# Kernel optimization log

Measured on AMD Instinct MI355X. Metric: run time of the kernel, lower is better.

## Reference

```python
import jax, jax.numpy as jnp
import numpy as np

N_SEARCH, B, C, H, W = 10, 32, 768, 24, 24
HT, WT = 8, 8
HEADS, POOL = 12, 4


def _G(t):
    # Integral of the bilinear triangle kernel: G(t) = int_{-1}^{t} max(0,1-|s|) ds
    tc = jnp.clip(t, -1.0, 1.0)
    return 0.5 + tc * (1.0 - 0.5 * jnp.abs(tc))


def prroi_pool(feats, rois, pool):
    # feats: [R,C,H,W], rois: [R,4] pixel coords (x0,y0,x1,y1); exact PrRoIPool2D
    R, C_, H_, W_ = feats.shape
    x0, y0, x1, y1 = rois[:, 0], rois[:, 1], rois[:, 2], rois[:, 3]
    bw = (x1 - x0) / pool
    bh = (y1 - y0) / pool
    p = jnp.arange(pool, dtype=feats.dtype)
    ex0 = x0[:, None] + p[None, :] * bw[:, None]   # [R,pool]
    ex1 = ex0 + bw[:, None]
    ey0 = y0[:, None] + p[None, :] * bh[:, None]
    ey1 = ey0 + bh[:, None]
    ix = jnp.arange(W_, dtype=feats.dtype)
    iy = jnp.arange(H_, dtype=feats.dtype)
    wx = _G(ex1[:, :, None] - ix) - _G(ex0[:, :, None] - ix)  # [R,pool,W]
    wy = _G(ey1[:, :, None] - iy) - _G(ey0[:, :, None] - iy)  # [R,pool,H]
    area = jnp.maximum(bw * bh, 1e-8)[:, None, None, None]
    return jnp.einsum('rph,rqw,rchw->rcpq', wy, wx, feats) / area  # [R,C,pool,pool]


def layernorm(x, g, b, eps=1e-5):
    m = jnp.mean(x, -1, keepdims=True)
    v = jnp.mean((x - m) ** 2, -1, keepdims=True)
    return (x - m) * jax.lax.rsqrt(v + eps) * g + b


def setup_inputs():
    key = jax.random.key(0)
    ks = jax.random.split(key, 24)
    search_feats = jax.random.normal(ks[0], (N_SEARCH, B, C, H, W), jnp.float32)
    template_feat = jax.random.normal(ks[1], (N_SEARCH, B, C, HT, WT), jnp.float32)
    u = jax.random.uniform(ks[2], (N_SEARCH, B, 4), jnp.float32)
    x0 = 0.05 + 0.4 * u[..., 0]
    y0 = 0.05 + 0.4 * u[..., 1]
    x1 = x0 + 0.15 + 0.3 * u[..., 2]
    y1 = y0 + 0.15 + 0.3 * u[..., 3]
    search_boxes = jnp.stack([x0, y0, x1, y1], -1)  # normalized, x1>x0, y1>y0
    s = 0.02
    d = {
        'search_feats': search_feats,
        'template_feat': template_feat,
        'search_boxes': search_boxes,
        'score_token': s * jax.random.normal(ks[3], (1, 1, C), jnp.float32),
        'ln1_g': jnp.ones((C,), jnp.float32), 'ln1_b': jnp.zeros((C,), jnp.float32),
        'Wq': s * jax.random.normal(ks[4], (2, C, C), jnp.float32), 'bq': jnp.zeros((2, C), jnp.float32),
        'Wk': s * jax.random.normal(ks[5], (2, C, C), jnp.float32), 'bk': jnp.zeros((2, C), jnp.float32),
        'Wv': s * jax.random.normal(ks[6], (2, C, C), jnp.float32), 'bv': jnp.zeros((2, C), jnp.float32),
        'Wo': s * jax.random.normal(ks[7], (2, C, C), jnp.float32), 'bo': jnp.zeros((2, C), jnp.float32),
        'ln2_g': jnp.ones((2, C), jnp.float32), 'ln2_b': jnp.zeros((2, C), jnp.float32),
        'Wmix': s * jax.random.normal(ks[8], (2, N_SEARCH, N_SEARCH), jnp.float32),
        'bmix': jnp.zeros((2, N_SEARCH), jnp.float32),
        'W1': s * jax.random.normal(ks[9], (C, C), jnp.float32), 'b1': jnp.zeros((C,), jnp.float32),
        'W2': s * jax.random.normal(ks[10], (C, C), jnp.float32), 'b2': jnp.zeros((C,), jnp.float32),
        'W3': s * jax.random.normal(ks[11], (C, 1), jnp.float32), 'b3': jnp.zeros((1,), jnp.float32),
    }
    return d


def reference(search_feats, template_feat, search_boxes, score_token, ln1_g, ln1_b,
              Wq, bq, Wk, bk, Wv, bv, Wo, bo, ln2_g, ln2_b, Wmix, bmix,
              W1, b1, W2, b2, W3, b3):
    N, b, c, h, w = search_feats.shape
    heads, pool = HEADS, POOL
    dh = c // heads
    scale = c ** (-0.5)  # note: full hidden_dim scale, as in original

    boxes = (search_boxes * w).reshape(-1, 4)              # [N*b,4] pixel coords
    feats = search_feats.reshape(-1, c, h, w)              # [N*b,c,h,w]
    pooled = prroi_pool(feats, boxes, pool)                # [N*b,c,pool,pool]
    # 'b c h w -> b (h w) c' then split N
    sbf = pooled.reshape(N, b, c, pool * pool).transpose(0, 1, 3, 2)  # [N,b,16,c]
    tmpl = template_feat.reshape(N, b, c, -1).transpose(0, 1, 3, 2)   # [N,b,64,c]

    x = jnp.broadcast_to(score_token, (N, b, 1, c))
    x = layernorm(x, ln1_g, ln1_b)
    kv = [sbf, tmpl]
    for i in range(2):
        q = x @ Wq[i] + bq[i]                              # [N,b,1,c]
        k = kv[i] @ Wk[i] + bk[i]                          # [N,b,T,c]
        v = kv[i] @ Wv[i] + bv[i]
        T = k.shape[2]
        qh = q.reshape(N, b, 1, heads, dh).transpose(0, 1, 3, 2, 4)   # [N,b,H,1,d]
        kh = k.reshape(N, b, T, heads, dh).transpose(0, 1, 3, 2, 4)   # [N,b,H,T,d]
        vh = v.reshape(N, b, T, heads, dh).transpose(0, 1, 3, 2, 4)
        attn = jax.nn.softmax(jnp.einsum('nbhld,nbhtd->nbhlt', qh, kh) * scale, -1)
        o = jnp.einsum('nbhlt,nbhtd->nbhld', attn, vh)
        o = o.transpose(0, 1, 3, 2, 4).reshape(N, b, 1, c)
        o = layernorm(o @ Wo[i] + bo[i], ln2_g[i], ln2_b[i])
        # time-mix across the N frames: [N,b,1,c] -> [b,c,N] -> linear -> [N,b,1,c]
        t = o[:, :, 0, :].transpose(1, 2, 0)               # [b,c,N]
        t = t @ Wmix[i] + bmix[i]
        x = t.transpose(2, 0, 1)[:, :, None, :]            # [N,b,1,c]

    hdd = jax.nn.relu(x @ W1 + b1)
    hdd = jax.nn.relu(hdd @ W2 + b2)
    return hdd @ W3 + b3                                   # [N,b,1,1]
```

## Files before the change

### kernel.cpp

```cpp
#include <hip/hip_runtime.h>
#include <cstdint>
#include <cstddef>

namespace {

constexpr float kScale = 0.03608439182435161f;
constexpr float kEps   = 1e-5f;

constexpr size_t OFF_QK0T = 0;
constexpr size_t OFF_QBK0 = 9216;
constexpr size_t OFF_S    = 16384;
constexpr size_t OFF_QK1  = OFF_S   + 2949120;
constexpr size_t OFF_O    = OFF_QK1 + 2949120;
constexpr size_t OFF_U    = OFF_O   + 245760;
constexpr size_t OFF_X    = OFF_U   + 245760;
constexpr size_t OFF_QF1  = OFF_X   + 245760;
constexpr size_t OFF_H1   = OFF_QF1 + 245760;
constexpr size_t OFF_H2   = OFF_H1  + 245760;
constexpr size_t OFF_WF   = OFF_H2  + 245760;
constexpr size_t WF_MAT_SHORTS = 1179648;
constexpr size_t OFF_P    = OFF_WF + (7*WF_MAT_SHORTS)/2;

typedef short short8v __attribute__((ext_vector_type(8)));
typedef float float4v __attribute__((ext_vector_type(4)));

union BP  { int4 i4; short8v s8; };
union S4P { int2 i2; short s[4]; };

__device__ __forceinline__ void splitBf(float a, short &h, short &l){
    unsigned u = __float_as_uint(a);
    h = (short)(u >> 16);
    float r = a - __uint_as_float(u & 0xFFFF0000u);
    l = (short)(__float_as_uint(r) >> 16);
}

__device__ __forceinline__ float Gf(float t){
    float tc = fminf(fmaxf(t, -1.f), 1.f);
    return 0.5f + tc * (1.f - 0.5f * fabsf(tc));
}

__device__ __forceinline__ float blockReduce256(float v, float* red){
    #pragma unroll
    for (int off = 1; off < 64; off <<= 1) v += __shfl_xor(v, off);
    __syncthreads();
    if ((threadIdx.x & 63) == 0) red[threadIdx.x >> 6] = v;
    __syncthreads();
    return red[0] + red[1] + red[2] + red[3];
}

__global__ __launch_bounds__(256) void k_wprep(
        const float* __restrict__ w0, const float* __restrict__ w1,
        const float* __restrict__ w2, const float* __restrict__ w3,
        const float* __restrict__ w4, const float* __restrict__ w5,
        const float* __restrict__ w6, short* __restrict__ WF){
    const float* Wsel[7] = {w0,w1,w2,w3,w4,w5,w6};
    const float* W = Wsel[blockIdx.y];
    const int unit = blockIdx.x * 4 + (threadIdx.x >> 6);
    const int l = threadIdx.x & 63;
    const int kt = unit / 48, nb = unit % 48;
    const int n = nb*16 + (l & 15);
    const int kb = kt*32 + ((l >> 4) << 2);
    S4P hi0, hi1, lo0, lo1;
    #pragma unroll
    for (int e = 0; e < 4; ++e){
        float a = W[(size_t)(kb + e) * 768 + n];
        splitBf(a, hi0.s[e], lo0.s[e]);
        float b = W[(size_t)(kb + 16 + e) * 768 + n];
        splitBf(b, hi1.s[e], lo1.s[e]);
    }
    size_t base = (size_t)blockIdx.y * WF_MAT_SHORTS + (size_t)unit * 1024 + (size_t)l * 8;
    *(int2*)(WF + base)            = hi0.i2;
    *(int2*)(WF + base + 4)        = hi1.i2;
    *(int2*)(WF + base + 512)      = lo0.i2;
    *(int2*)(WF + base + 512 + 4)  = lo1.i2;
}

template<int HG, int RELU>
__global__ __launch_bounds__(256) void k_mgemm(
        const float* __restrict__ A, const short* __restrict__ WFm,
        const float* __restrict__ bias, float* __restrict__ C){
    __shared__ short AF[2][2][64][8];
    const int h   = blockIdx.y;
    const int m0  = blockIdx.x * 16;
    const int tid = threadIdx.x;
    const int l   = tid & 63;
    const int w   = tid >> 6;

    const int srow = tid >> 3, sk4 = tid & 7;
    const int slane = srow + 16 * (sk4 & 3);
    const int sebase = 4 * (sk4 >> 2);
    const float* aRow = HG ? (A + ((size_t)(m0 + srow) * 12 + h) * 768)
                           : (A + (size_t)(m0 + srow) * 768);

    const int nb = h * 4 + w;
    const short* WB = WFm + (size_t)nb * 1024 + (size_t)l * 8;

    float4v acc = {0.f,0.f,0.f,0.f};

    if (tid < 128){
        float4 a0 = *(const float4*)(aRow + sk4 * 4);
        S4P hi, lo;
        splitBf(a0.x, hi.s[0], lo.s[0]); splitBf(a0.y, hi.s[1], lo.s[1]);
        splitBf(a0.z, hi.s[2], lo.s[2]); splitBf(a0.w, hi.s[3], lo.s[3]);
        *(int2*)&AF[0][0][slane][sebase] = hi.i2;
        *(int2*)&AF[0][1][slane][sebase] = lo.i2;
    }
    BP bh, bl;
    bh.i4 = *(const int4*)(WB);
    bl.i4 = *(const int4*)(WB + 512);
    __syncthreads();

    #pragma unroll 1
    for (int kt = 0; kt < 24; ++kt){
        const int cur = kt & 1;
        const int ktn = (kt < 23) ? kt + 1 : 23;
        float4 aN;
        if (tid < 128) aN = *(const float4*)(aRow + ktn * 32 + sk4 * 4);
        BP cbh = bh, cbl = bl;
        {
            const short* wb = WB + (size_t)ktn * 49152;
            bh.i4 = *(const int4*)(wb);
            bl.i4 = *(const int4*)(wb + 512);
        }
        short8v ah = *(short8v*)&AF[cur][0][l][0];
        short8v al = *(short8v*)&AF[cur][1][l][0];
        acc = __builtin_amdgcn_mfma_f32_16x16x32_bf16(ah, cbh.s8, acc, 0, 0, 0);
        acc = __builtin_amdgcn_mfma_f32_16x16x32_bf16(al, cbh.s8, acc, 0, 0, 0);
        acc = __builtin_amdgcn_mfma_f32_16x16x32_bf16(ah, cbl.s8, acc, 0, 0, 0);
        if (kt < 23 && tid < 128){
            S4P hi, lo;
            splitBf(aN.x, hi.s[0], lo.s[0]); splitBf(aN.y, hi.s[1], lo.s[1]);
            splitBf(aN.z, hi.s[2], lo.s[2]); splitBf(aN.w, hi.s[3], lo.s[3]);
            *(int2*)&AF[cur ^ 1][0][slane][sebase] = hi.i2;
            *(int2*)&AF[cur ^ 1][1][slane][sebase] = lo.i2;
        }
        __syncthreads();
    }

    const int col = h * 64 + w * 16 + (l & 15);
    const float bb = bias[col];
    #pragma unroll
    for (int reg = 0; reg < 4; ++reg){
        int row = m0 + ((l >> 4) << 2) + reg;
        float v = acc[reg] + bb;
        if (RELU) v = fmaxf(v, 0.f);
        C[(size_t)row * 768 + col] = v;
    }
}

__global__ __launch_bounds__(256) void k_prep(
        const float* __restrict__ token, const float* __restrict__ g1,
        const float* __restrict__ b1,    const float* __restrict__ Wq0,
        const float* __restrict__ bq0,   const float* __restrict__ Wk0,
        const float* __restrict__ bk0,
        float* __restrict__ qk0T, float* __restrict__ qbk0){
    __shared__ float x0l[768];
    __shared__ float red[8];
    __shared__ float qfp[4][64];
    __shared__ float qfl[64];
    __shared__ float Ws[64][68];
    const int h  = blockIdx.x / 12;
    const int ct = blockIdx.x % 12;
    const int tid = threadIdx.x;

    float v0 = token[tid], v1 = token[tid+256], v2 = token[tid+512];
    float s = blockReduce256(v0+v1+v2, red);
    float m = s * (1.f/768.f);
    float d0 = v0-m, d1 = v1-m, d2 = v2-m;
    float qv = blockReduce256(d0*d0+d1*d1+d2*d2, red);
    float rs = rsqrtf(qv*(1.f/768.f) + kEps);
    x0l[tid]     = d0*rs*g1[tid]     + b1[tid];
    x0l[tid+256] = d1*rs*g1[tid+256] + b1[tid+256];
    x0l[tid+512] = d2*rs*g1[tid+512] + b1[tid+512];
    __syncthreads();

    {
        int dl = tid & 63, part = tid >> 6;
        int d = h*64 + dl;
        float a = 0.f;
        for (int c = part*192; c < part*192 + 192; ++c)
            a += x0l[c] * Wq0[(size_t)c*768 + d];
        qfp[part][dl] = a;
    }
    __syncthreads();
    if (tid < 64){
        int d = h*64 + tid;
        qfl[tid] = qfp[0][tid]+qfp[1][tid]+qfp[2][tid]+qfp[3][tid] + bq0[d];
    }
    __syncthreads();
    if (ct == 0 && tid < 64){
        float v = qfl[tid] * bk0[h*64 + tid];
        #pragma unroll
        for (int off = 1; off < 64; off <<= 1) v += __shfl_xor(v, off);
        if (tid == 0) qbk0[h] = v;
    }
    #pragma unroll
    for (int i = 0; i < 4; ++i){
        int f = tid + i*256; int cl = f >> 4, dd = (f & 15)*4;
        float4 v = *(const float4*)(Wk0 + (size_t)(ct*64+cl)*768 + h*64 + dd);
        *(float4*)&Ws[cl][dd] = v;
    }
    __syncthreads();
    {
        int cl = tid >> 2, part = tid & 3;
        float a = 0.f;
        #pragma unroll
        for (int jj = 0; jj < 16; ++jj){
            int dd = part*16 + jj;
            a += Ws[cl][dd] * qfl[dd];
        }
        a += __shfl_xor(a, 1); a += __shfl_xor(a, 2);
        if (part == 0) qk0T[h*768 + ct*64 + cl] = a;
    }
}

__global__ __launch_bounds__(256) void k_pool2(
        const float* __restrict__ feats, const float* __restrict__ boxes,
        float* __restrict__ P){
    __shared__ float Xs[32*580];
    __shared__ float wxp[24][4];
    __shared__ float wyp[24][4];
    __shared__ int   rng[2];
    __shared__ float areaInvS;
    const int r = blockIdx.x, cc = blockIdx.y * 32, tid = threadIdx.x;

    float bx0 = boxes[r*4+0]*24.f, by0 = boxes[r*4+1]*24.f;
    float bx1 = boxes[r*4+2]*24.f, by1 = boxes[r*4+3]*24.f;
    float bw = (bx1-bx0)*0.25f, bh = (by1-by0)*0.25f;
    if (tid == 0){
        int hlo = (int)floorf(by0) - 1; if (hlo < 0) hlo = 0;
        int hhi = (int)floorf(by1) + 1; if (hhi > 23) hhi = 23;
        rng[0] = hlo; rng[1] = hhi - hlo + 1;
        areaInvS = 1.f / fmaxf(bw*bh, 1e-8f);
    }
    if (tid < 24){
        int w = tid;
        #pragma unroll
        for (int q = 0; q < 4; ++q){
            float e0 = bx0 + q*bw, e1 = e0 + bw;
            wxp[w][q] = Gf(e1 - (float)w) - Gf(e0 - (float)w);
        }
    } else if (tid < 48){
        int hh = tid - 24;
        #pragma unroll
        for (int p = 0; p < 4; ++p){
            float e0 = by0 + p*bh, e1 = e0 + bh;
            wyp[hh][p] = Gf(e1 - (float)hh) - Gf(e0 - (float)hh);
        }
    }
    __syncthreads();
    const int hlo = rng[0], nr = rng[1];
    const float aInv = areaInvS;

    const int nf4 = nr * 192;
    for (int idx = tid; idx < nf4; idx += 256){
        int ri  = idx / 192;
        int rem = idx - ri * 192;
        int cl  = rem / 6;
        int w4  = rem - cl * 6;
        float4 v = *(const float4*)(feats + ((size_t)(r*768 + cc + cl))*576
                                    + (hlo + ri)*24 + w4*4);
        *(float4*)&Xs[cl*580 + ri*24 + w4*4] = v;
    }
    __syncthreads();

    const int j = tid & 7;
    const int cl = tid >> 3;
    float acc[16];
    #pragma unroll
    for (int k = 0; k < 16; ++k) acc[k] = 0.f;
    for (int ri = j; ri < nr; ri += 8){
        const float* xr = &Xs[cl*580 + ri*24];
        float z[4] = {0.f,0.f,0.f,0.f};
        #pragma unroll
        for (int w4 = 0; w4 < 6; ++w4){
            float4 xv = *(const float4*)(xr + w4*4);
            float xa[4] = {xv.x, xv.y, xv.z, xv.w};
            #pragma unroll
            for (int k = 0; k < 4; ++k){
                float4 wv = *(const float4*)&wxp[w4*4+k][0];
                z[0] += wv.x*xa[k]; z[1] += wv.y*xa[k];
                z[2] += wv.z*xa[k]; z[3] += wv.w*xa[k];
            }
        }
        float4 wyv = *(const float4*)&wyp[hlo+ri][0];
        float wya[4] = {wyv.x, wyv.y, wyv.z, wyv.w};
        #pragma unroll
        for (int p = 0; p < 4; ++p)
            #pragma unroll
            for (int q = 0; q < 4; ++q)
                acc[p*4+q] += wya[p]*z[q];
    }
    #pragma unroll
    for (int k = 0; k < 16; ++k){
        acc[k] += __shfl_xor(acc[k], 1);
        acc[k] += __shfl_xor(acc[k], 2);
        acc[k] += __shfl_xor(acc[k], 4);
    }
    float o0 = acc[0], o1 = acc[8];
    #pragma unroll
    for (int k = 1; k < 8; ++k){
        if (j == k){ o0 = acc[k]; o1 = acc[k+8]; }
    }
    P[((size_t)r*16 + j)*768 + cc + cl]     = o0 * aInv;
    P[((size_t)r*16 + j + 8)*768 + cc + cl] = o1 * aInv;
}

__global__ __launch_bounds__(256) void k_attn0(
        const float* __restrict__ P, const float* __restrict__ qk0T,
        const float* __restrict__ qbk0g, float* __restrict__ s0){
    __shared__ float P2[16][776];
    __shared__ float logitsL[12][17];
    __shared__ float attnT[16][12];
    const int r = blockIdx.x, tid = threadIdx.x;

    #pragma unroll
    for (int i = 0; i < 12; ++i){
        int f = tid + i*256;
        int t = f / 192, c4 = f - t*192;
        float4 v = *(const float4*)(P + ((size_t)r*16 + t)*768 + c4*4);
        *(float4*)&P2[t][c4*4] = v;
    }
    __syncthreads();

    if (tid < 192){
        int h = tid >> 4, t = tid & 15;
        float a = qbk0g[h];
        const float* qrow = qk0T + h*768;
        #pragma unroll 4
        for (int c4 = 0; c4 < 192; ++c4){
            float4 qv = *(const float4*)(qrow + c4*4);
            float4 pv = *(const float4*)&P2[t][c4*4];
            a += qv.x*pv.x + qv.y*pv.y + qv.z*pv.z + qv.w*pv.w;
        }
        logitsL[h][t] = a * kScale;
    }
    __syncthreads();
    if (tid < 12){
        float mx = -1e30f;
        for (int t = 0; t < 16; ++t) mx = fmaxf(mx, logitsL[tid][t]);
        float ss = 0.f;
        for (int t = 0; t < 16; ++t){
            float e = expf(logitsL[tid][t] - mx);
            attnT[t][tid] = e; ss += e;
        }
        float rsn = 1.f/ss;
        for (int t = 0; t < 16; ++t) attnT[t][tid] *= rsn;
    }
    __syncthreads();
    #pragma unroll
    for (int s3 = 0; s3 < 3; ++s3){
        int c = tid + s3*256;
        float a12[12];
        #pragma unroll
        for (int h = 0; h < 12; ++h) a12[h] = 0.f;
        #pragma unroll
        for (int t = 0; t < 16; ++t){
            float x = P2[t][c];
            float4 a0 = *(const float4*)&attnT[t][0];
            float4 a1 = *(const float4*)&attnT[t][4];
            float4 a2 = *(const float4*)&attnT[t][8];
            a12[0] += a0.x*x; a12[1] += a0.y*x; a12[2]  += a0.z*x; a12[3]  += a0.w*x;
            a12[4] += a1.x*x; a12[5] += a1.y*x; a12[6]  += a1.z*x; a12[7]  += a1.w*x;
            a12[8] += a2.x*x; a12[9] += a2.y*x; a12[10] += a2.z*x; a12[11] += a2.w*x;
        }
        #pragma unroll
        for (int h = 0; h < 12; ++h)
            s0[((size_t)r*12 + h)*768 + c] = a12[h];
    }
}

__global__ __launch_bounds__(256) void k_qk1(
        const float* __restrict__ qf1, const float* __restrict__ Wk1,
        float* __restrict__ qk1){
    __shared__ float As[32][68];
    __shared__ float Bs[64][68];
    const int r0 = blockIdx.x * 32, h = blockIdx.y, c0 = blockIdx.z * 64;
    const int tid = threadIdx.x;
    #pragma unroll
    for (int i = 0; i < 2; ++i){
        int f = tid + i*256; int ml = f >> 4, kk = (f & 15)*4;
        *(float4*)&As[ml][kk] =
            *(const float4*)(qf1 + (size_t)(r0+ml)*768 + h*64 + kk);
    }
    #pragma unroll
    for (int i = 0; i < 4; ++i){
        int f = tid + i*256; int cl = f >> 4, dd = (f & 15)*4;
        float4 v = *(const float4*)(Wk1 + (size_t)(c0+cl)*768 + h*64 + dd);
        Bs[dd+0][cl] = v.x; Bs[dd+1][cl] = v.y;
        Bs[dd+2][cl] = v.z; Bs[dd+3][cl] = v.w;
    }
    __syncthreads();
    const int tn = tid & 15, tm = tid >> 4;
    float acc0[4] = {0.f,0.f,0.f,0.f};
    float acc1[4] = {0.f,0.f,0.f,0.f};
    #pragma unroll
    for (int k4 = 0; k4 < 16; ++k4){
        float4 av0 = *(const float4*)&As[tm*2+0][k4*4];
        float4 av1 = *(const float4*)&As[tm*2+1][k4*4];
        float a0a[4] = {av0.x, av0.y, av0.z, av0.w};
        float a1a[4] = {av1.x, av1.y, av1.z, av1.w};
        #pragma unroll
        for (int jj = 0; jj < 4; ++jj){
            float4 bv = *(const float4*)&Bs[k4*4+jj][tn*4];
            acc0[0] += a0a[jj]*bv.x; acc0[1] += a0a[jj]*bv.y;
            acc0[2] += a0a[jj]*bv.z; acc0[3] += a0a[jj]*bv.w;
            acc1[0] += a1a[jj]*bv.x; acc1[1] += a1a[jj]*bv.y;
            acc1[2] += a1a[jj]*bv.z; acc1[3] += a1a[jj]*bv.w;
        }
    }
    float4 o0; o0.x=acc0[0]; o0.y=acc0[1]; o0.z=acc0[2]; o0.w=acc0[3];
    float4 o1; o1.x=acc1[0]; o1.y=acc1[1]; o1.z=acc1[2]; o1.w=acc1[3];
    *(float4*)(qk1 + ((size_t)(r0+tm*2+0)*12 + h)*768 + c0 + tn*4) = o0;
    *(float4*)(qk1 + ((size_t)(r0+tm*2+1)*12 + h)*768 + c0 + tn*4) = o1;
}

__global__ __launch_bounds__(256) void k_attn1(
        const float* __restrict__ tmpl, const float* __restrict__ qf1,
        const float* __restrict__ bk1,  const float* __restrict__ qk1,
        float* __restrict__ s1){
    __shared__ float Tc[192][68];
    __shared__ float logitsT[64][13];
    __shared__ float attnH[12][64];
    __shared__ float qbk[12];
    const int r = blockIdx.x, tid = threadIdx.x;
    const float* tp = tmpl + (size_t)r*768*64;

    if (tid < 192){
        int h = tid >> 4, pp = tid & 15;
        float v = 0.f;
        #pragma unroll
        for (int jj = 0; jj < 4; ++jj){
            int d = h*64 + pp*4 + jj;
            v += bk1[d] * qf1[(size_t)r*768 + d];
        }
        v += __shfl_xor(v,1); v += __shfl_xor(v,2);
        v += __shfl_xor(v,4); v += __shfl_xor(v,8);
        if (pp == 0) qbk[h] = v;
    }
    __syncthreads();
    float lacc[3];
    #pragma unroll
    for (int s = 0; s < 3; ++s){
        int task = tid + s*256;
        lacc[s] = qbk[task >> 6];
    }
    for (int cb = 0; cb < 4; ++cb){
        #pragma unroll
        for (int i = 0; i < 12; ++i){
            int f = tid + i*256; int cl = f >> 4, t4 = (f & 15)*4;
            *(float4*)&Tc[cl][t4] =
                *(const float4*)(tp + (size_t)(cb*192 + cl)*64 + t4);
        }
        __syncthreads();
        #pragma unroll
        for (int s = 0; s < 3; ++s){
            int task = tid + s*256;
            int h = task >> 6, t = task & 63;
            const float* qrow = qk1 + ((size_t)r*12 + h)*768 + cb*192;
            float a = 0.f;
            #pragma unroll 4
            for (int c4 = 0; c4 < 48; ++c4){
                float4 qv = *(const float4*)(qrow + c4*4);
                a += qv.x*Tc[c4*4+0][t] + qv.y*Tc[c4*4+1][t]
                   + qv.z*Tc[c4*4+2][t] + qv.w*Tc[c4*4+3][t];
            }
            lacc[s] += a;
        }
        __syncthreads();
    }
    #pragma unroll
    for (int s = 0; s < 3; ++s){
        int task = tid + s*256;
        logitsT[task & 63][task >> 6] = lacc[s] * kScale;
    }
    __syncthreads();
    if (tid < 12){
        float mx = -1e30f;
        for (int t = 0; t < 64; ++t) mx = fmaxf(mx, logitsT[t][tid]);
        float ss = 0.f;
        for (int t = 0; t < 64; ++t){
            float e = expf(logitsT[t][tid] - mx);
            attnH[tid][t] = e; ss += e;
        }
        float rsn = 1.f/ss;
        for (int t = 0; t < 64; ++t) attnH[tid][t] *= rsn;
    }
    __syncthreads();
    for (int cb = 0; cb < 4; ++cb){
        #pragma unroll
        for (int i = 0; i < 12; ++i){
            int f = tid + i*256; int cl = f >> 4, t4 = (f & 15)*4;
            *(float4*)&Tc[cl][t4] =
                *(const float4*)(tp + (size_t)(cb*192 + cl)*64 + t4);
        }
        __syncthreads();
        if (tid < 192){
            float4 trow[16];
            #pragma unroll
            for (int t4 = 0; t4 < 16; ++t4)
                trow[t4] = *(const float4*)&Tc[tid][t4*4];
            int c = cb*192 + tid;
            #pragma unroll
            for (int h = 0; h < 12; ++h){
                float a = 0.f;
                #pragma unroll
                for (int t4 = 0; t4 < 16; ++t4){
                    float4 avv = *(const float4*)&attnH[h][t4*4];
                    float4 tv = trow[t4];
                    a += avv.x*tv.x + avv.y*tv.y + avv.z*tv.z + avv.w*tv.w;
                }
                s1[((size_t)r*12 + h)*768 + c] = a;
            }
        }
        __syncthreads();
    }
}

__global__ __launch_bounds__(256) void k_lnmix(
        const float* __restrict__ u, const float* __restrict__ g,
        const float* __restrict__ bta, const float* __restrict__ Wmix,
        const float* __restrict__ bmix, float* __restrict__ xout){
    __shared__ float lnl[10][768];
    __shared__ float red[8];
    __shared__ float wm[100];
    __shared__ float bm[10];
    const int b = blockIdx.x, tid = threadIdx.x;
    if (tid < 100) wm[tid] = Wmix[tid];
    if (tid < 10)  bm[tid] = bmix[tid];
    for (int n = 0; n < 10; ++n){
        const float* row = u + (size_t)(n*32 + b)*768;
        float v0 = row[tid], v1 = row[tid+256], v2 = row[tid+512];
        float s = blockReduce256(v0+v1+v2, red);
        float m = s * (1.f/768.f);
        float d0 = v0-m, d1 = v1-m, d2 = v2-m;
        float qv = blockReduce256(d0*d0+d1*d1+d2*d2, red);
        float rs = rsqrtf(qv*(1.f/768.f) + kEps);
        lnl[n][tid]     = d0*rs*g[tid]     + bta[tid];
        lnl[n][tid+256] = d1*rs*g[tid+256] + bta[tid+256];
        lnl[n][tid+512] = d2*rs*g[tid+512] + bta[tid+512];
    }
    __syncthreads();
    #pragma unroll
    for (int s3 = 0; s3 < 3; ++s3){
        int c = tid + s3*256;
        float col[10];
        #pragma unroll
        for (int n = 0; n < 10; ++n) col[n] = lnl[n][c];
        #pragma unroll
        for (int np = 0; np < 10; ++np){
            float a = bm[np];
            #pragma unroll
            for (int n = 0; n < 10; ++n) a += col[n]*wm[n*10+np];
            xout[(size_t)(np*32 + b)*768 + c] = a;
        }
    }
}

__global__ __launch_bounds__(256) void k_head(
        const float* __restrict__ h2v, const float* __restrict__ W3,
        const float* __restrict__ b3, float* __restrict__ out){
    __shared__ float red[8];
    const int r = blockIdx.x, tid = threadIdx.x;
    const float* row = h2v + (size_t)r*768;
    float a = row[tid]*W3[tid] + row[tid+256]*W3[tid+256] + row[tid+512]*W3[tid+512];
    a = blockReduce256(a, red);
    if (tid == 0) out[r] = a + b3[0];
}

}

extern "C" void kernel_launch(void* const* d_in, const int* in_sizes, int n_in,
                              void* d_out, int out_size, void* d_ws, size_t ws_size,
                              hipStream_t stream){
    const float* feats = (const float*)d_in[0];
    const float* tmpl  = (const float*)d_in[1];
    const float* boxes = (const float*)d_in[2];
    const float* token = (const float*)d_in[3];
    const float* ln1g  = (const float*)d_in[4];
    const float* ln1b  = (const float*)d_in[5];
    const float* Wq    = (const float*)d_in[6];
    const float* bq    = (const float*)d_in[7];
    const float* Wk    = (const float*)d_in[8];
    const float* bk    = (const float*)d_in[9];
    const float* Wv    = (const float*)d_in[10];
    const float* bv    = (const float*)d_in[11];
    const float* Wo    = (const float*)d_in[12];
    const float* bo    = (const float*)d_in[13];
    const float* ln2g  = (const float*)d_in[14];
    const float* ln2b  = (const float*)d_in[15];
    const float* Wmix  = (const float*)d_in[16];
    const float* bmix  = (const float*)d_in[17];
    const float* W1    = (const float*)d_in[18];
    const float* b1v   = (const float*)d_in[19];
    const float* W2    = (const float*)d_in[20];
    const float* b2v   = (const float*)d_in[21];
    const float* W3    = (const float*)d_in[22];
    const float* b3v   = (const float*)d_in[23];
    float* ws  = (float*)d_ws;
    float* out = (float*)d_out;

    float* qk0T = ws + OFF_QK0T;
    float* qbk0 = ws + OFF_QBK0;
    float* sbuf = ws + OFF_S;
    float* qk1  = ws + OFF_QK1;
    float* obuf = ws + OFF_O;
    float* ubuf = ws + OFF_U;
    float* xbuf = ws + OFF_X;
    float* qf1  = ws + OFF_QF1;
    float* h1b  = ws + OFF_H1;
    float* h2b  = ws + OFF_H2;
    short* wf   = (short*)(ws + OFF_WF);
    float* Pbuf = ws + OFF_P;

    const size_t MO = 589824;
    short* wfv0 = wf + 0*WF_MAT_SHORTS;
    short* wfo0 = wf + 1*WF_MAT_SHORTS;
    short* wfq1 = wf + 2*WF_MAT_SHORTS;
    short* wfv1 = wf + 3*WF_MAT_SHORTS;
    short* wfo1 = wf + 4*WF_MAT_SHORTS;
    short* wf1  = wf + 5*WF_MAT_SHORTS;
    short* wf2  = wf + 6*WF_MAT_SHORTS;

    k_wprep<<<dim3(288,7), 256, 0, stream>>>(Wv, Wo, Wq + MO, Wv + MO, Wo + MO, W1, W2, wf);
    k_prep<<<144, 256, 0, stream>>>(token, ln1g, ln1b, Wq, bq, Wk, bk, qk0T, qbk0);
    k_pool2<<<dim3(320,24), 256, 0, stream>>>(feats, boxes, Pbuf);
    k_attn0<<<320, 256, 0, stream>>>(Pbuf, qk0T, qbk0, sbuf);
    k_mgemm<1,0><<<dim3(20,12), 256, 0, stream>>>(sbuf, wfv0, bv, obuf);
    k_mgemm<0,0><<<dim3(20,12), 256, 0, stream>>>(obuf, wfo0, bo, ubuf);
    k_lnmix<<<32, 256, 0, stream>>>(ubuf, ln2g, ln2b, Wmix, bmix, xbuf);
    k_mgemm<0,0><<<dim3(20,12), 256, 0, stream>>>(xbuf, wfq1, bq + 768, qf1);
    k_qk1<<<dim3(10,12,12), 256, 0, stream>>>(qf1, Wk + MO, qk1);
    k_attn1<<<320, 256, 0, stream>>>(tmpl, qf1, bk + 768, qk1, sbuf);
    k_mgemm<1,0><<<dim3(20,12), 256, 0, stream>>>(sbuf, wfv1, bv + 768, obuf);
    k_mgemm<0,0><<<dim3(20,12), 256, 0, stream>>>(obuf, wfo1, bo + 768, ubuf);
    k_lnmix<<<32, 256, 0, stream>>>(ubuf, ln2g + 768, ln2b + 768, Wmix + 100, bmix + 10, xbuf);
    k_mgemm<0,1><<<dim3(20,12), 256, 0, stream>>>(xbuf, wf1, b1v, h1b);
    k_mgemm<0,1><<<dim3(20,12), 256, 0, stream>>>(h1b, wf2, b2v, h2b);
    k_head<<<320, 256, 0, stream>>>(h2b, W3, b3v, out);
}
```

Before: 404.3 us.

## Merge weight prep with token prep, retile mgemm, shrink pool2 LDS

Fuses the weight-splitting kernel and the token/query prep kernel into one launch that dispatches on block index. The split-bf16 GEMM is retiled to 32 rows per block with 8 waves and a K-step of 64, halving the grid and sharing each weight fragment across two row tiles. pool2 now stages rows in chunks of 12 instead of the full window, which cuts LDS per block for occupancy at the cost of extra barriers. Together these target launch overhead, weight re-reads and LDS-limited occupancy.

After: 363.3 us. 1.11x faster.

```diff
diff --git a/kernel.cpp b/kernel.cpp
--- a/kernel.cpp
+++ b/kernel.cpp
@@ -48,107 +48,11 @@
     return red[0] + red[1] + red[2] + red[3];
 }
 
-__global__ __launch_bounds__(256) void k_wprep(
+__global__ __launch_bounds__(256) void k_prepall(
         const float* __restrict__ w0, const float* __restrict__ w1,
         const float* __restrict__ w2, const float* __restrict__ w3,
         const float* __restrict__ w4, const float* __restrict__ w5,
-        const float* __restrict__ w6, short* __restrict__ WF){
-    const float* Wsel[7] = {w0,w1,w2,w3,w4,w5,w6};
-    const float* W = Wsel[blockIdx.y];
-    const int unit = blockIdx.x * 4 + (threadIdx.x >> 6);
-    const int l = threadIdx.x & 63;
-    const int kt = unit / 48, nb = unit % 48;
-    const int n = nb*16 + (l & 15);
-    const int kb = kt*32 + ((l >> 4) << 2);
-    S4P hi0, hi1, lo0, lo1;
-    #pragma unroll
-    for (int e = 0; e < 4; ++e){
-        float a = W[(size_t)(kb + e) * 768 + n];
-        splitBf(a, hi0.s[e], lo0.s[e]);
-        float b = W[(size_t)(kb + 16 + e) * 768 + n];
-        splitBf(b, hi1.s[e], lo1.s[e]);
-    }
-    size_t base = (size_t)blockIdx.y * WF_MAT_SHORTS + (size_t)unit * 1024 + (size_t)l * 8;
-    *(int2*)(WF + base)            = hi0.i2;
-    *(int2*)(WF + base + 4)        = hi1.i2;
-    *(int2*)(WF + base + 512)      = lo0.i2;
-    *(int2*)(WF + base + 512 + 4)  = lo1.i2;
-}
-
-template<int HG, int RELU>
-__global__ __launch_bounds__(256) void k_mgemm(
-        const float* __restrict__ A, const short* __restrict__ WFm,
-        const float* __restrict__ bias, float* __restrict__ C){
-    __shared__ short AF[2][2][64][8];
-    const int h   = blockIdx.y;
-    const int m0  = blockIdx.x * 16;
-    const int tid = threadIdx.x;
-    const int l   = tid & 63;
-    const int w   = tid >> 6;
-
-    const int srow = tid >> 3, sk4 = tid & 7;
-    const int slane = srow + 16 * (sk4 & 3);
-    const int sebase = 4 * (sk4 >> 2);
-    const float* aRow = HG ? (A + ((size_t)(m0 + srow) * 12 + h) * 768)
-                           : (A + (size_t)(m0 + srow) * 768);
-
-    const int nb = h * 4 + w;
-    const short* WB = WFm + (size_t)nb * 1024 + (size_t)l * 8;
-
-    float4v acc = {0.f,0.f,0.f,0.f};
-
-    if (tid < 128){
-        float4 a0 = *(const float4*)(aRow + sk4 * 4);
-        S4P hi, lo;
-        splitBf(a0.x, hi.s[0], lo.s[0]); splitBf(a0.y, hi.s[1], lo.s[1]);
-        splitBf(a0.z, hi.s[2], lo.s[2]); splitBf(a0.w, hi.s[3], lo.s[3]);
-        *(int2*)&AF[0][0][slane][sebase] = hi.i2;
-        *(int2*)&AF[0][1][slane][sebase] = lo.i2;
-    }
-    BP bh, bl;
-    bh.i4 = *(const int4*)(WB);
-    bl.i4 = *(const int4*)(WB + 512);
-    __syncthreads();
-
-    #pragma unroll 1
-    for (int kt = 0; kt < 24; ++kt){
-        const int cur = kt & 1;
-        const int ktn = (kt < 23) ? kt + 1 : 23;
-        float4 aN;
-        if (tid < 128) aN = *(const float4*)(aRow + ktn * 32 + sk4 * 4);
-        BP cbh = bh, cbl = bl;
-        {
-            const short* wb = WB + (size_t)ktn * 49152;
-            bh.i4 = *(const int4*)(wb);
-            bl.i4 = *(const int4*)(wb + 512);
-        }
-        short8v ah = *(short8v*)&AF[cur][0][l][0];
-        short8v al = *(short8v*)&AF[cur][1][l][0];
-        acc = __builtin_amdgcn_mfma_f32_16x16x32_bf16(ah, cbh.s8, acc, 0, 0, 0);
-        acc = __builtin_amdgcn_mfma_f32_16x16x32_bf16(al, cbh.s8, acc, 0, 0, 0);
-        acc = __builtin_amdgcn_mfma_f32_16x16x32_bf16(ah, cbl.s8, acc, 0, 0, 0);
-        if (kt < 23 && tid < 128){
-            S4P hi, lo;
-            splitBf(aN.x, hi.s[0], lo.s[0]); splitBf(aN.y, hi.s[1], lo.s[1]);
-            splitBf(aN.z, hi.s[2], lo.s[2]); splitBf(aN.w, hi.s[3], lo.s[3]);
-            *(int2*)&AF[cur ^ 1][0][slane][sebase] = hi.i2;
-            *(int2*)&AF[cur ^ 1][1][slane][sebase] = lo.i2;
-        }
-        __syncthreads();
-    }
-
-    const int col = h * 64 + w * 16 + (l & 15);
-    const float bb = bias[col];
-    #pragma unroll
-    for (int reg = 0; reg < 4; ++reg){
-        int row = m0 + ((l >> 4) << 2) + reg;
-        float v = acc[reg] + bb;
-        if (RELU) v = fmaxf(v, 0.f);
-        C[(size_t)row * 768 + col] = v;
-    }
-}
-
-__global__ __launch_bounds__(256) void k_prep(
+        const float* __restrict__ w6, short* __restrict__ WF,
         const float* __restrict__ token, const float* __restrict__ g1,
         const float* __restrict__ b1,    const float* __restrict__ Wq0,
         const float* __restrict__ bq0,   const float* __restrict__ Wk0,
@@ -159,9 +63,38 @@
     __shared__ float qfp[4][64];
     __shared__ float qfl[64];
     __shared__ float Ws[64][68];
-    const int h  = blockIdx.x / 12;
-    const int ct = blockIdx.x % 12;
+    const int gb = blockIdx.x;
     const int tid = threadIdx.x;
+    const int l = tid & 63;
+
+    if (gb < 2016){
+        const float* Wsel[7] = {w0,w1,w2,w3,w4,w5,w6};
+        const int mat = gb / 288;
+        const int bxx = gb - mat*288;
+        const float* W = Wsel[mat];
+        const int unit = bxx * 4 + (tid >> 6);
+        const int kt = unit / 48, nb = unit % 48;
+        const int n = nb*16 + (l & 15);
+        const int kb = kt*32 + ((l >> 4) << 2);
+        S4P hi0, hi1, lo0, lo1;
+        #pragma unroll
+        for (int e = 0; e < 4; ++e){
+            float a = W[(size_t)(kb + e) * 768 + n];
+            splitBf(a, hi0.s[e], lo0.s[e]);
+            float b = W[(size_t)(kb + 16 + e) * 768 + n];
+            splitBf(b, hi1.s[e], lo1.s[e]);
+        }
+        size_t base = (size_t)mat * WF_MAT_SHORTS + (size_t)unit * 1024 + (size_t)l * 8;
+        *(int2*)(WF + base)            = hi0.i2;
+        *(int2*)(WF + base + 4)        = hi1.i2;
+        *(int2*)(WF + base + 512)      = lo0.i2;
+        *(int2*)(WF + base + 512 + 4)  = lo1.i2;
+        return;
+    }
+
+    const int pb = gb - 2016;
+    const int h  = pb / 12;
+    const int ct = pb % 12;
 
     float v0 = token[tid], v1 = token[tid+256], v2 = token[tid+512];
     float s = blockReduce256(v0+v1+v2, red);
@@ -214,10 +147,96 @@
     }
 }
 
+template<int HG, int RELU>
+__global__ __launch_bounds__(512) void k_mgemm(
+        const float* __restrict__ A, const short* __restrict__ WFm,
+        const float* __restrict__ bias, float* __restrict__ C){
+    __shared__ short AF[2][2][2][2][64][8];
+    const int h   = blockIdx.y;
+    const int m0  = blockIdx.x * 32;
+    const int tid = threadIdx.x;
+    const int l   = tid & 63;
+    const int w   = tid >> 6;
+    const int wm  = w >> 2, wn = w & 3;
+
+    const int srow = tid >> 4;
+    const int sk4  = tid & 15;
+    const int sfs  = sk4 >> 3;
+    const int ss   = sk4 & 7;
+    const int sfm  = srow >> 4;
+    const int slane = (srow & 15) + 16 * (ss & 3);
+    const int seb   = 4 * (ss >> 2);
+    const float* aRow = HG ? (A + ((size_t)(m0 + srow) * 12 + h) * 768)
+                           : (A + (size_t)(m0 + srow) * 768);
+
+    const int nb = h * 4 + wn;
+    const short* WB = WFm + (size_t)nb * 1024 + (size_t)l * 8;
+
+    float4v acc = {0.f,0.f,0.f,0.f};
+
+    {
+        float4 a0 = *(const float4*)(aRow + sk4 * 4);
+        S4P hi, lo;
+        splitBf(a0.x, hi.s[0], lo.s[0]); splitBf(a0.y, hi.s[1], lo.s[1]);
+        splitBf(a0.z, hi.s[2], lo.s[2]); splitBf(a0.w, hi.s[3], lo.s[3]);
+        *(int2*)&AF[0][sfs][sfm][0][slane][seb] = hi.i2;
+        *(int2*)&AF[0][sfs][sfm][1][slane][seb] = lo.i2;
+    }
+    BP bh0, bl0, bh1, bl1;
+    bh0.i4 = *(const int4*)(WB);
+    bl0.i4 = *(const int4*)(WB + 512);
+    bh1.i4 = *(const int4*)(WB + 49152);
+    bl1.i4 = *(const int4*)(WB + 49152 + 512);
+    __syncthreads();
+
+    #pragma unroll 1
+    for (int kt = 0; kt < 12; ++kt){
+        const int cur = kt & 1;
+        float4 aN;
+        if (kt < 11) aN = *(const float4*)(aRow + (kt+1) * 64 + sk4 * 4);
+        BP cbh0 = bh0, cbl0 = bl0, cbh1 = bh1, cbl1 = bl1;
+        if (kt < 11){
+            const short* wb = WB + (size_t)(2*kt + 2) * 49152;
+            bh0.i4 = *(const int4*)(wb);
+            bl0.i4 = *(const int4*)(wb + 512);
+            bh1.i4 = *(const int4*)(wb + 49152);
+            bl1.i4 = *(const int4*)(wb + 49152 + 512);
+        }
+        short8v ah0 = *(short8v*)&AF[cur][0][wm][0][l][0];
+        short8v al0 = *(short8v*)&AF[cur][0][wm][1][l][0];
+        short8v ah1 = *(short8v*)&AF[cur][1][wm][0][l][0];
+        short8v al1 = *(short8v*)&AF[cur][1][wm][1][l][0];
+        acc = __builtin_amdgcn_mfma_f32_16x16x32_bf16(ah0, cbh0.s8, acc, 0, 0, 0);
+        acc = __builtin_amdgcn_mfma_f32_16x16x32_bf16(al0, cbh0.s8, acc, 0, 0, 0);
+        acc = __builtin_amdgcn_mfma_f32_16x16x32_bf16(ah0, cbl0.s8, acc, 0, 0, 0);
+        acc = __builtin_amdgcn_mfma_f32_16x16x32_bf16(ah1, cbh1.s8, acc, 0, 0, 0);
+        acc = __builtin_amdgcn_mfma_f32_16x16x32_bf16(al1, cbh1.s8, acc, 0, 0, 0);
+        acc = __builtin_amdgcn_mfma_f32_16x16x32_bf16(ah1, cbl1.s8, acc, 0, 0, 0);
+        if (kt < 11){
+            S4P hi, lo;
+            splitBf(aN.x, hi.s[0], lo.s[0]); splitBf(aN.y, hi.s[1], lo.s[1]);
+            splitBf(aN.z, hi.s[2], lo.s[2]); splitBf(aN.w, hi.s[3], lo.s[3]);
+            *(int2*)&AF[cur ^ 1][sfs][sfm][0][slane][seb] = hi.i2;
+            *(int2*)&AF[cur ^ 1][sfs][sfm][1][slane][seb] = lo.i2;
+        }
+        __syncthreads();
+    }
+
+    const int col = h * 64 + wn * 16 + (l & 15);
+    const float bb = bias[col];
+    #pragma unroll
+    for (int reg = 0; reg < 4; ++reg){
+        int row = m0 + wm * 16 + ((l >> 4) << 2) + reg;
+        float v = acc[reg] + bb;
+        if (RELU) v = fmaxf(v, 0.f);
+        C[(size_t)row * 768 + col] = v;
+    }
+}
+
 __global__ __launch_bounds__(256) void k_pool2(
         const float* __restrict__ feats, const float* __restrict__ boxes,
         float* __restrict__ P){
-    __shared__ float Xs[32*580];
+    __shared__ float Xs[32*292];
     __shared__ float wxp[24][4];
     __shared__ float wyp[24][4];
     __shared__ int   rng[2];
@@ -251,45 +270,49 @@
     __syncthreads();
     const int hlo = rng[0], nr = rng[1];
     const float aInv = areaInvS;
-
-    const int nf4 = nr * 192;
-    for (int idx = tid; idx < nf4; idx += 256){
-        int ri  = idx / 192;
-        int rem = idx - ri * 192;
-        int cl  = rem / 6;
-        int w4  = rem - cl * 6;
-        float4 v = *(const float4*)(feats + ((size_t)(r*768 + cc + cl))*576
-                                    + (hlo + ri)*24 + w4*4);
-        *(float4*)&Xs[cl*580 + ri*24 + w4*4] = v;
-    }
-    __syncthreads();
-
     const int j = tid & 7;
     const int cl = tid >> 3;
+
     float acc[16];
     #pragma unroll
     for (int k = 0; k < 16; ++k) acc[k] = 0.f;
-    for (int ri = j; ri < nr; ri += 8){
-        const float* xr = &Xs[cl*580 + ri*24];
-        float z[4] = {0.f,0.f,0.f,0.f};
-        #pragma unroll
-        for (int w4 = 0; w4 < 6; ++w4){
-            float4 xv = *(const float4*)(xr + w4*4);
-            float xa[4] = {xv.x, xv.y, xv.z, xv.w};
+
+    for (int rb = 0; rb < nr; rb += 12){
+        const int nrl = (nr - rb < 12) ? (nr - rb) : 12;
+        const int nf4 = nrl * 192;
+        __syncthreads();
+        for (int idx = tid; idx < nf4; idx += 256){
+            int ri  = idx / 192;
+            int rem = idx - ri * 192;
+            int c2  = rem / 6;
+            int w4  = rem - c2 * 6;
+            float4 v = *(const float4*)(feats + ((size_t)(r*768 + cc + c2))*576
+                                        + (hlo + rb + ri)*24 + w4*4);
+            *(float4*)&Xs[c2*292 + ri*24 + w4*4] = v;
+        }
+        __syncthreads();
+        for (int rl = j; rl < nrl; rl += 8){
+            const float* xr = &Xs[cl*292 + rl*24];
+            float z[4] = {0.f,0.f,0.f,0.f};
             #pragma unroll
-            for (int k = 0; k < 4; ++k){
-                float4 wv = *(const float4*)&wxp[w4*4+k][0];
-                z[0] += wv.x*xa[k]; z[1] += wv.y*xa[k];
-                z[2] += wv.z*xa[k]; z[3] += wv.w*xa[k];
+            for (int w4 = 0; w4 < 6; ++w4){
+                float4 xv = *(const float4*)(xr + w4*4);
+                float xa[4] = {xv.x, xv.y, xv.z, xv.w};
+                #pragma unroll
+                for (int k = 0; k < 4; ++k){
+                    float4 wv = *(const float4*)&wxp[w4*4+k][0];
+                    z[0] += wv.x*xa[k]; z[1] += wv.y*xa[k];
+                    z[2] += wv.z*xa[k]; z[3] += wv.w*xa[k];
+                }
             }
-        }
-        float4 wyv = *(const float4*)&wyp[hlo+ri][0];
-        float wya[4] = {wyv.x, wyv.y, wyv.z, wyv.w};
-        #pragma unroll
-        for (int p = 0; p < 4; ++p)
+            float4 wyv = *(const float4*)&wyp[hlo+rb+rl][0];
+            float wya[4] = {wyv.x, wyv.y, wyv.z, wyv.w};
             #pragma unroll
-            for (int q = 0; q < 4; ++q)
-                acc[p*4+q] += wya[p]*z[q];
+            for (int p = 0; p < 4; ++p)
+                #pragma unroll
+                for (int q = 0; q < 4; ++q)
+                    acc[p*4+q] += wya[p]*z[q];
+        }
     }
     #pragma unroll
     for (int k = 0; k < 16; ++k){
@@ -622,20 +645,20 @@
     short* wf1  = wf + 5*WF_MAT_SHORTS;
     short* wf2  = wf + 6*WF_MAT_SHORTS;
 
-    k_wprep<<<dim3(288,7), 256, 0, stream>>>(Wv, Wo, Wq + MO, Wv + MO, Wo + MO, W1, W2, wf);
-    k_prep<<<144, 256, 0, stream>>>(token, ln1g, ln1b, Wq, bq, Wk, bk, qk0T, qbk0);
+    k_prepall<<<2160, 256, 0, stream>>>(Wv, Wo, Wq + MO, Wv + MO, Wo + MO, W1, W2, wf,
+                                        token, ln1g, ln1b, Wq, bq, Wk, bk, qk0T, qbk0);
     k_pool2<<<dim3(320,24), 256, 0, stream>>>(feats, boxes, Pbuf);
     k_attn0<<<320, 256, 0, stream>>>(Pbuf, qk0T, qbk0, sbuf);
-    k_mgemm<1,0><<<dim3(20,12), 256, 0, stream>>>(sbuf, wfv0, bv, obuf);
-    k_mgemm<0,0><<<dim3(20,12), 256, 0, stream>>>(obuf, wfo0, bo, ubuf);
+    k_mgemm<1,0><<<dim3(10,12), 512, 0, stream>>>(sbuf, wfv0, bv, obuf);
+    k_mgemm<0,0><<<dim3(10,12), 512, 0, stream>>>(obuf, wfo0, bo, ubuf);
     k_lnmix<<<32, 256, 0, stream>>>(ubuf, ln2g, ln2b, Wmix, bmix, xbuf);
-    k_mgemm<0,0><<<dim3(20,12), 256, 0, stream>>>(xbuf, wfq1, bq + 768, qf1);
+    k_mgemm<0,0><<<dim3(10,12), 512, 0, stream>>>(xbuf, wfq1, bq + 768, qf1);
     k_qk1<<<dim3(10,12,12), 256, 0, stream>>>(qf1, Wk + MO, qk1);
     k_attn1<<<320, 256, 0, stream>>>(tmpl, qf1, bk + 768, qk1, sbuf);
-    k_mgemm<1,0><<<dim3(20,12), 256, 0, stream>>>(sbuf, wfv1, bv + 768, obuf);
-    k_mgemm<0,0><<<dim3(20,12), 256, 0, stream>>>(obuf, wfo1, bo + 768, ubuf);
+    k_mgemm<1,0><<<dim3(10,12), 512, 0, stream>>>(sbuf, wfv1, bv + 768, obuf);
+    k_mgemm<0,0><<<dim3(10,12), 512, 0, stream>>>(obuf, wfo1, bo + 768, ubuf);
     k_lnmix<<<32, 256, 0, stream>>>(ubuf, ln2g + 768, ln2b + 768, Wmix + 100, bmix + 10, xbuf);
-    k_mgemm<0,1><<<dim3(20,12), 256, 0, stream>>>(xbuf, wf1, b1v, h1b);
-    k_mgemm<0,1><<<dim3(20,12), 256, 0, stream>>>(h1b, wf2, b2v, h2b);
+    k_mgemm<0,1><<<dim3(10,12), 512, 0, stream>>>(xbuf, wf1, b1v, h1b);
+    k_mgemm<0,1><<<dim3(10,12), 512, 0, stream>>>(h1b, wf2, b2v, h2b);
     k_head<<<320, 256, 0, stream>>>(h2b, W3, b3v, out);
 }
```
